# Kernel tuning notes

Measured on AMD Instinct MI355X. Metric: run time of the kernel, lower is better.

## Reference

```python
import jax, jax.numpy as jnp
import numpy as np

VAL = 1.0  # shift weight value

def shift_plus(x, val=VAL):
    """Per-channel-group spatial shift ('+' mode), equivalent to the
    groups=C 3x3 conv with a single nonzero tap per channel, padding=1.
    x: [B, C, H, W], C % 5 == 0.
    """
    c = x.shape[1]
    cgp = c // 5
    xp = jnp.pad(x, ((0, 0), (0, 0), (1, 1), (1, 1)))
    g0 = xp[:, 0 * cgp:1 * cgp, 1:-1, 2:]    # tap (1,2): pull from w+1
    g1 = xp[:, 1 * cgp:2 * cgp, 1:-1, :-2]   # tap (1,0): pull from w-1
    g2 = xp[:, 2 * cgp:3 * cgp, 2:, 1:-1]    # tap (2,1): pull from h+1
    g3 = xp[:, 3 * cgp:4 * cgp, :-2, 1:-1]   # tap (0,1): pull from h-1
    g4 = x[:, 4 * cgp:, :, :]                # tap (1,1): identity
    return jnp.concatenate([g0, g1, g2, g3, g4], axis=1) * val

def shift_conv1x1(x, w, b):
    # shift then pointwise conv (1x1) with bias
    xs = shift_plus(x)
    y = jnp.einsum('bchw,oc->bohw', xs, w)
    return y + b[None, :, None, None]

def setup_inputs() -> dict:
    key = jax.random.key(0)
    k1, k2, k3, k4, k5 = jax.random.split(key, 5)
    B, Cin, H, W = 8, 100, 256, 256
    Chid, Cout = 200, 100
    x = jax.random.normal(k1, (B, Cin, H, W), dtype=jnp.float32)
    w1 = jax.random.normal(k2, (Chid, Cin), dtype=jnp.float32) * 0.02
    b1 = jax.random.normal(k3, (Chid,), dtype=jnp.float32) * 0.02
    w2 = jax.random.normal(k4, (Cout, Chid), dtype=jnp.float32) * 0.02
    b2 = jax.random.normal(k5, (Cout,), dtype=jnp.float32) * 0.02
    return {"x": x, "w1": w1, "b1": b1, "w2": w2, "b2": b2}

def reference(x, w1, b1, w2, b2):
    h = shift_conv1x1(x, w1, b1)
    h = jax.nn.gelu(h, approximate=False)  # torch nn.GELU default is exact erf
    return shift_conv1x1(h, w2, b2)
```

## Files before the change

### kernel.cpp

```cpp
#include <hip/hip_runtime.h>
#include <math.h>

typedef unsigned short u16;
typedef unsigned int   u32;
typedef short bf16x8 __attribute__((ext_vector_type(8)));
typedef float f32x4  __attribute__((ext_vector_type(4)));

__device__ __forceinline__ u16 f2bf(float f) {
  u32 u = __builtin_bit_cast(u32, f);
  u32 r = (u + 0x7fffu + ((u >> 16) & 1u)) >> 16;
  return (u16)r;
}
__device__ __forceinline__ float gelu_exact(float v) {
  return 0.5f * v * (1.0f + erff(v * 0.70710678118654752f));
}

#define H_BYTES   209715200ll
#define FW1_ELEMS 26624
#define FW2_ELEMS 25088

__global__ void prep_frags(const float* __restrict__ w1, const float* __restrict__ w2,
                           u16* __restrict__ fw1, u16* __restrict__ fw2) {
  int gid = blockIdx.x * 256 + threadIdx.x;
  if (gid < FW1_ELEMS) {
    int j = gid & 7, lane = (gid >> 3) & 63, rest = gid >> 9;
    int nt = rest % 13, kc = rest / 13;
    int c = kc * 32 + (lane >> 4) * 8 + j;
    int o = nt * 16 + (lane & 15);
    float v = (c < 100 && o < 200) ? w1[o * 100 + c] : 0.f;
    fw1[gid] = f2bf(v);
  } else if (gid < FW1_ELEMS + FW2_ELEMS) {
    int i2 = gid - FW1_ELEMS;
    int j = i2 & 7, lane = (i2 >> 3) & 63, rest = i2 >> 9;
    int nt = rest % 7, kc = rest / 7;
    int c = kc * 32 + (lane >> 4) * 8 + j;
    int o = nt * 16 + (lane & 15);
    float v = (c < 200 && o < 100) ? w2[o * 200 + c] : 0.f;
    fw2[i2] = f2bf(v);
  }
}

#define SK1  136
#define SKO1 208
__global__ __launch_bounds__(256, 4) void conv1_kernel(
    const float* __restrict__ x, const u16* __restrict__ fw1,
    const float* __restrict__ b1, u16* __restrict__ hbuf) {
  __shared__ __align__(16) char smem[64 * SKO1 * 2];
  u16* At = (u16*)smem;
  u16* Ot = (u16*)smem;
  const int t   = threadIdx.x;
  const int bid = blockIdx.x;
  const int bx  = ((bid & 7) << 10) | (bid >> 3);
  const int b  = bx >> 10;
  const int hh = (bx >> 2) & 255;
  const int w0 = (bx & 3) << 6;

  {
    const int m  = t & 63;
    const int kh = t >> 6;
    const int wp = w0 + m;
    #pragma unroll
    for (int g = 0; g < 4; ++g) {
      const int c0 = 8 * (kh + 4 * g);
      if (c0 >= 100) {
        *(uint4*)&At[m * SK1 + c0] = make_uint4(0u, 0u, 0u, 0u);
        continue;
      }
      u32 pk[4];
      #pragma unroll
      for (int jj = 0; jj < 8; ++jj) {
        const int c = c0 + jj;
        float v = 0.f;
        if (c < 100) {
          const int dw = (c < 20) ? 1 : ((c < 40) ? -1 : 0);
          const int dh = (c >= 40 && c < 60) ? 1 : ((c >= 60 && c < 80) ? -1 : 0);
          const int hs = hh + dh, ws = wp + dw;
          if ((unsigned)hs < 256u && (unsigned)ws < 256u)
            v = x[((b * 100 + c) * 256 + hs) * 256 + ws];
        }
        const u32 bv = f2bf(v);
        if (jj & 1) pk[jj >> 1] |= bv << 16; else pk[jj >> 1] = bv;
      }
      *(uint4*)&At[m * SK1 + c0] = make_uint4(pk[0], pk[1], pk[2], pk[3]);
    }
  }
  __syncthreads();

  const int lane = t & 63, wid = t >> 6;
  const int col = lane & 15, q = lane >> 4;
  f32x4 acc[13];
  #pragma unroll
  for (int nt = 0; nt < 13; ++nt) acc[nt] = (f32x4)0.0f;

  const bf16x8* wf = (const bf16x8*)fw1 + lane;
  #pragma unroll 1
  for (int kc = 0; kc < 4; ++kc) {
    const bf16x8 a = *(const bf16x8*)&At[(wid * 16 + col) * SK1 + kc * 32 + q * 8];
    #pragma unroll
    for (int nt = 0; nt < 13; ++nt) {
      const bf16x8 bf = wf[(kc * 13 + nt) * 64];
      acc[nt] = __builtin_amdgcn_mfma_f32_16x16x32_bf16(bf, a, acc[nt], 0, 0, 0);
    }
  }

  __syncthreads();

  #pragma unroll
  for (int nt = 0; nt < 13; ++nt) {
    const int ob = nt * 16 + 4 * q;
    const float4 bias4 = (ob <= 196) ? *(const float4*)&b1[ob]
                                     : make_float4(0.f, 0.f, 0.f, 0.f);
    const f32x4 v = acc[nt];
    const int px = wid * 16 + col;
    const u32 p0 = (u32)f2bf(gelu_exact(v[0] + bias4.x)) |
                   ((u32)f2bf(gelu_exact(v[1] + bias4.y)) << 16);
    const u32 p1 = (u32)f2bf(gelu_exact(v[2] + bias4.z)) |
                   ((u32)f2bf(gelu_exact(v[3] + bias4.w)) << 16);
    *(uint2*)&Ot[px * SKO1 + ob] = make_uint2(p0, p1);
  }
  __syncthreads();
  {
    const int rowbase = ((b * 256 + hh) * 256 + w0) * 200;
    #pragma unroll
    for (int s = 0; s < 7; ++s) {
      const int id = s * 256 + t;
      if (id < 1600) {
        const int px = id / 25;
        const int ch = id - px * 25;
        const uint4 d = *(const uint4*)&Ot[px * SKO1 + ch * 8];
        *(uint4*)&hbuf[rowbase + px * 200 + ch * 8] = d;
      }
    }
  }
}

#define SK2 232
#define PS2 68
__global__ __launch_bounds__(256, 4) void conv2_kernel(
    const u16* __restrict__ hbuf, const u16* __restrict__ fw2,
    const float* __restrict__ b2, float* __restrict__ out) {
  __shared__ __align__(16) char smem[112 * PS2 * 4];
  u16*   At = (u16*)smem;
  float* Ob = (float*)smem;
  const int t   = threadIdx.x;
  const int bid = blockIdx.x;
  const int bx  = ((bid & 7) << 10) | (bid >> 3);
  const int b  = bx >> 10;
  const int hh = (bx >> 2) & 255;
  const int w0 = (bx & 3) << 6;

  {
    const int m  = t & 63;
    const int kh = t >> 6;
    const int wp = w0 + m;
    #pragma unroll
    for (int g = 0; g < 7; ++g) {
      const int c0 = 8 * (kh + 4 * g);
      if (c0 >= 200) {
        *(uint4*)&At[m * SK2 + c0] = make_uint4(0u, 0u, 0u, 0u);
        continue;
      }
      const int dw = (c0 < 40) ? 1 : ((c0 < 80) ? -1 : 0);
      const int dh = (c0 >= 80 && c0 < 120) ? 1 : ((c0 >= 120 && c0 < 160) ? -1 : 0);
      const int hs = hh + dh, ws = wp + dw;
      const bool ok = ((unsigned)hs < 256u) && ((unsigned)ws < 256u);
      const int hsc = ok ? hs : hh;
      const int wsc = ok ? ws : wp;
      uint4 d = *(const uint4*)&hbuf[((b * 256 + hsc) * 256 + wsc) * 200 + c0];
      if (!ok) d = make_uint4(0u, 0u, 0u, 0u);
      *(uint4*)&At[m * SK2 + c0] = d;
    }
  }
  __syncthreads();

  const int lane = t & 63, wid = t >> 6;
  const int col = lane & 15, q = lane >> 4;
  f32x4 acc[7];
  #pragma unroll
  for (int nt = 0; nt < 7; ++nt) acc[nt] = (f32x4)0.0f;

  const bf16x8* wf = (const bf16x8*)fw2 + lane;
  #pragma unroll 1
  for (int kc = 0; kc < 7; ++kc) {
    const bf16x8 a = *(const bf16x8*)&At[(wid * 16 + col) * SK2 + kc * 32 + q * 8];
    #pragma unroll
    for (int nt = 0; nt < 7; ++nt) {
      const bf16x8 bf = wf[(kc * 7 + nt) * 64];
      acc[nt] = __builtin_amdgcn_mfma_f32_16x16x32_bf16(a, bf, acc[nt], 0, 0, 0);
    }
  }

  __syncthreads();

  #pragma unroll
  for (int nt = 0; nt < 7; ++nt) {
    const int o = nt * 16 + col;
    const float bias = (o < 100) ? b2[o] : 0.f;
    const f32x4 v = acc[nt];
    *(float4*)&Ob[o * PS2 + wid * 16 + 4 * q] =
        make_float4(v[0] + bias, v[1] + bias, v[2] + bias, v[3] + bias);
  }
  __syncthreads();
  {
    const int obase = b * 6553600 + hh * 256 + w0;
    #pragma unroll
    for (int s = 0; s < 7; ++s) {
      const int id = s * 256 + t;
      if (id < 1600) {
        const int oo = id >> 4, ch = id & 15;
        const float4 d = *(const float4*)&Ob[oo * PS2 + ch * 4];
        *(float4*)&out[obase + oo * 65536 + ch * 4] = d;
      }
    }
  }
}

extern "C" void kernel_launch(void* const* d_in, const int* in_sizes, int n_in,
                              void* d_out, int out_size, void* d_ws, size_t ws_size,
                              hipStream_t stream) {
  const float* x  = (const float*)d_in[0];
  const float* w1 = (const float*)d_in[1];
  const float* b1 = (const float*)d_in[2];
  const float* w2 = (const float*)d_in[3];
  const float* b2 = (const float*)d_in[4];
  float* out = (float*)d_out;

  u16* hbuf = (u16*)d_ws;
  u16* fw1  = (u16*)((char*)d_ws + H_BYTES);
  u16* fw2  = (u16*)((char*)d_ws + H_BYTES + FW1_ELEMS * 2);

  prep_frags<<<202, 256, 0, stream>>>(w1, w2, fw1, fw2);
  conv1_kernel<<<8192, 256, 0, stream>>>(x, fw1, b1, hbuf);
  conv2_kernel<<<8192, 256, 0, stream>>>(hbuf, fw2, b2, out);
}
```

Baseline: 576.3 us.

## Load MFMA A-fragments directly into registers and use fast GELU approximation

Both conv kernels now gather their shifted input straight from global memory into MFMA A-fragment registers instead of staging through LDS, removing shared-memory round trips and barriers. conv1 also writes its GELU output directly to global memory, skipping the LDS transpose. Exact erf-based GELU is replaced by an Abramowitz-Stegun polynomial with fast exp and reciprocal, and bf16 packing uses the v_cvt_pk_bf16_f32 instruction. The risks are less-coalesced global access patterns (uint2 stores strided by 400 bytes per pixel, scalar x loads) and a small accuracy loss from the approximated erf.

Result: slower. 615.1 us (+6.7%).

```diff
diff --git a/kernel.cpp b/kernel.cpp
--- a/kernel.cpp
+++ b/kernel.cpp
@@ -11,8 +11,22 @@
   u32 r = (u + 0x7fffu + ((u >> 16) & 1u)) >> 16;
   return (u16)r;
 }
-__device__ __forceinline__ float gelu_exact(float v) {
-  return 0.5f * v * (1.0f + erff(v * 0.70710678118654752f));
+__device__ __forceinline__ u32 pkbf(float lo, float hi) {
+  u32 r;
+  asm("v_cvt_pk_bf16_f32 %0, %1, %2" : "=v"(r) : "v"(lo), "v"(hi));
+  return r;
+}
+__device__ __forceinline__ float gelu_fast(float v) {
+  const float xa = fabsf(v) * 0.70710678118654752f;
+  const float t  = __builtin_amdgcn_rcpf(fmaf(0.3275911f, xa, 1.0f));
+  float p = fmaf(1.061405429f, t, -1.453152027f);
+  p = fmaf(p, t, 1.421413741f);
+  p = fmaf(p, t, -0.284496736f);
+  p = fmaf(p, t, 0.254829592f);
+  p = p * t;
+  const float e  = __expf(-xa * xa);
+  const float g  = 0.5f * v * (p * e);
+  return (v >= 0.f) ? (v - g) : g;
 }
 
 #define H_BYTES   209715200ll
@@ -40,14 +54,22 @@
   }
 }
 
-#define SK1  136
-#define SKO1 208
+__device__ __forceinline__ float loadx(const float* __restrict__ x,
+                                       int b, int hh, int wp, int c) {
+  float v = 0.f;
+  if (c < 100) {
+    const int dw = (c < 20) ? 1 : ((c < 40) ? -1 : 0);
+    const int dh = (c >= 40 && c < 60) ? 1 : ((c >= 60 && c < 80) ? -1 : 0);
+    const int hs = hh + dh, ws = wp + dw;
+    if ((unsigned)hs < 256u && (unsigned)ws < 256u)
+      v = x[((b * 100 + c) * 256 + hs) * 256 + ws];
+  }
+  return v;
+}
+
 __global__ __launch_bounds__(256, 4) void conv1_kernel(
     const float* __restrict__ x, const u16* __restrict__ fw1,
     const float* __restrict__ b1, u16* __restrict__ hbuf) {
-  __shared__ __align__(16) char smem[64 * SKO1 * 2];
-  u16* At = (u16*)smem;
-  u16* Ot = (u16*)smem;
   const int t   = threadIdx.x;
   const int bid = blockIdx.x;
   const int bx  = ((bid & 7) << 10) | (bid >> 3);
@@ -55,47 +77,32 @@
   const int hh = (bx >> 2) & 255;
   const int w0 = (bx & 3) << 6;
 
-  {
-    const int m  = t & 63;
-    const int kh = t >> 6;
-    const int wp = w0 + m;
-    #pragma unroll
-    for (int g = 0; g < 4; ++g) {
-      const int c0 = 8 * (kh + 4 * g);
-      if (c0 >= 100) {
-        *(uint4*)&At[m * SK1 + c0] = make_uint4(0u, 0u, 0u, 0u);
-        continue;
-      }
-      u32 pk[4];
-      #pragma unroll
-      for (int jj = 0; jj < 8; ++jj) {
-        const int c = c0 + jj;
-        float v = 0.f;
-        if (c < 100) {
-          const int dw = (c < 20) ? 1 : ((c < 40) ? -1 : 0);
-          const int dh = (c >= 40 && c < 60) ? 1 : ((c >= 60 && c < 80) ? -1 : 0);
-          const int hs = hh + dh, ws = wp + dw;
-          if ((unsigned)hs < 256u && (unsigned)ws < 256u)
-            v = x[((b * 100 + c) * 256 + hs) * 256 + ws];
-        }
-        const u32 bv = f2bf(v);
-        if (jj & 1) pk[jj >> 1] |= bv << 16; else pk[jj >> 1] = bv;
-      }
-      *(uint4*)&At[m * SK1 + c0] = make_uint4(pk[0], pk[1], pk[2], pk[3]);
-    }
-  }
-  __syncthreads();
-
   const int lane = t & 63, wid = t >> 6;
   const int col = lane & 15, q = lane >> 4;
+  const int px = w0 + wid * 16 + col;
+
+  uint4 aw[4];
+  #pragma unroll
+  for (int kc = 0; kc < 4; ++kc) {
+    u32 wd[4];
+    #pragma unroll
+    for (int p = 0; p < 4; ++p) {
+      const int c0 = kc * 32 + q * 8 + 2 * p;
+      const float v0 = loadx(x, b, hh, px, c0);
+      const float v1 = loadx(x, b, hh, px, c0 + 1);
+      wd[p] = pkbf(v0, v1);
+    }
+    aw[kc] = make_uint4(wd[0], wd[1], wd[2], wd[3]);
+  }
+
   f32x4 acc[13];
   #pragma unroll
   for (int nt = 0; nt < 13; ++nt) acc[nt] = (f32x4)0.0f;
 
   const bf16x8* wf = (const bf16x8*)fw1 + lane;
-  #pragma unroll 1
+  #pragma unroll
   for (int kc = 0; kc < 4; ++kc) {
-    const bf16x8 a = *(const bf16x8*)&At[(wid * 16 + col) * SK1 + kc * 32 + q * 8];
+    const bf16x8 a = __builtin_bit_cast(bf16x8, aw[kc]);
     #pragma unroll
     for (int nt = 0; nt < 13; ++nt) {
       const bf16x8 bf = wf[(kc * 13 + nt) * 64];
@@ -103,45 +110,25 @@
     }
   }
 
-  __syncthreads();
-
+  const int rowu = ((b * 256 + hh) * 256 + px) * 200;
   #pragma unroll
   for (int nt = 0; nt < 13; ++nt) {
     const int ob = nt * 16 + 4 * q;
-    const float4 bias4 = (ob <= 196) ? *(const float4*)&b1[ob]
-                                     : make_float4(0.f, 0.f, 0.f, 0.f);
-    const f32x4 v = acc[nt];
-    const int px = wid * 16 + col;
-    const u32 p0 = (u32)f2bf(gelu_exact(v[0] + bias4.x)) |
-                   ((u32)f2bf(gelu_exact(v[1] + bias4.y)) << 16);
-    const u32 p1 = (u32)f2bf(gelu_exact(v[2] + bias4.z)) |
-                   ((u32)f2bf(gelu_exact(v[3] + bias4.w)) << 16);
-    *(uint2*)&Ot[px * SKO1 + ob] = make_uint2(p0, p1);
-  }
-  __syncthreads();
-  {
-    const int rowbase = ((b * 256 + hh) * 256 + w0) * 200;
-    #pragma unroll
-    for (int s = 0; s < 7; ++s) {
-      const int id = s * 256 + t;
-      if (id < 1600) {
-        const int px = id / 25;
-        const int ch = id - px * 25;
-        const uint4 d = *(const uint4*)&Ot[px * SKO1 + ch * 8];
-        *(uint4*)&hbuf[rowbase + px * 200 + ch * 8] = d;
-      }
-    }
-  }
-}
-
-#define SK2 232
+    if (ob < 200) {
+      const float4 b4 = *(const float4*)&b1[ob];
+      const f32x4 v = acc[nt];
+      const u32 p0 = pkbf(gelu_fast(v[0] + b4.x), gelu_fast(v[1] + b4.y));
+      const u32 p1 = pkbf(gelu_fast(v[2] + b4.z), gelu_fast(v[3] + b4.w));
+      *(uint2*)&hbuf[rowu + ob] = make_uint2(p0, p1);
+    }
+  }
+}
+
 #define PS2 68
 __global__ __launch_bounds__(256, 4) void conv2_kernel(
     const u16* __restrict__ hbuf, const u16* __restrict__ fw2,
     const float* __restrict__ b2, float* __restrict__ out) {
-  __shared__ __align__(16) char smem[112 * PS2 * 4];
-  u16*   At = (u16*)smem;
-  float* Ob = (float*)smem;
+  __shared__ __align__(16) float Ob[112 * PS2];
   const int t   = threadIdx.x;
   const int bid = blockIdx.x;
   const int bx  = ((bid & 7) << 10) | (bid >> 3);
@@ -149,48 +136,42 @@
   const int hh = (bx >> 2) & 255;
   const int w0 = (bx & 3) << 6;
 
-  {
-    const int m  = t & 63;
-    const int kh = t >> 6;
-    const int wp = w0 + m;
-    #pragma unroll
-    for (int g = 0; g < 7; ++g) {
-      const int c0 = 8 * (kh + 4 * g);
-      if (c0 >= 200) {
-        *(uint4*)&At[m * SK2 + c0] = make_uint4(0u, 0u, 0u, 0u);
-        continue;
-      }
+  const int lane = t & 63, wid = t >> 6;
+  const int col = lane & 15, q = lane >> 4;
+  const int px = w0 + wid * 16 + col;
+
+  uint4 aw[7];
+  #pragma unroll
+  for (int kc = 0; kc < 7; ++kc) {
+    const int c0 = kc * 32 + q * 8;
+    uint4 d = make_uint4(0u, 0u, 0u, 0u);
+    if (c0 < 200) {
       const int dw = (c0 < 40) ? 1 : ((c0 < 80) ? -1 : 0);
       const int dh = (c0 >= 80 && c0 < 120) ? 1 : ((c0 >= 120 && c0 < 160) ? -1 : 0);
-      const int hs = hh + dh, ws = wp + dw;
+      const int hs = hh + dh, ws = px + dw;
       const bool ok = ((unsigned)hs < 256u) && ((unsigned)ws < 256u);
       const int hsc = ok ? hs : hh;
-      const int wsc = ok ? ws : wp;
-      uint4 d = *(const uint4*)&hbuf[((b * 256 + hsc) * 256 + wsc) * 200 + c0];
+      const int wsc = ok ? ws : px;
+      d = *(const uint4*)&hbuf[((b * 256 + hsc) * 256 + wsc) * 200 + c0];
       if (!ok) d = make_uint4(0u, 0u, 0u, 0u);
-      *(uint4*)&At[m * SK2 + c0] = d;
-    }
-  }
-  __syncthreads();
-
-  const int lane = t & 63, wid = t >> 6;
-  const int col = lane & 15, q = lane >> 4;
+    }
+    aw[kc] = d;
+  }
+
   f32x4 acc[7];
   #pragma unroll
   for (int nt = 0; nt < 7; ++nt) acc[nt] = (f32x4)0.0f;
 
   const bf16x8* wf = (const bf16x8*)fw2 + lane;
-  #pragma unroll 1
+  #pragma unroll
   for (int kc = 0; kc < 7; ++kc) {
-    const bf16x8 a = *(const bf16x8*)&At[(wid * 16 + col) * SK2 + kc * 32 + q * 8];
+    const bf16x8 a = __builtin_bit_cast(bf16x8, aw[kc]);
     #pragma unroll
     for (int nt = 0; nt < 7; ++nt) {
       const bf16x8 bf = wf[(kc * 7 + nt) * 64];
       acc[nt] = __builtin_amdgcn_mfma_f32_16x16x32_bf16(a, bf, acc[nt], 0, 0, 0);
     }
   }
-
-  __syncthreads();
 
   #pragma unroll
   for (int nt = 0; nt < 7; ++nt) {
```
